# Kernel tuning notes

Measured on AMD Instinct MI355X. Metric: run time of the kernel, lower is better.

Reference implementation:

```python
import jax, jax.numpy as jnp
import numpy as np
import math

NUM_HEADS = 16


def setup_inputs() -> dict:
    key = jax.random.key(0)
    ks = jax.random.split(key, 7)
    d_model = 2048
    b, s = 2, 2048
    h = NUM_HEADS
    dh = d_model // h
    past_len = 2048
    std = math.sqrt(2.0 / (d_model + d_model))
    def w(k):
        return std * jax.random.truncated_normal(k, -3.0, 3.0, (d_model, d_model), jnp.float32)
    return {
        "x": jax.random.normal(ks[0], (b, s, d_model), jnp.float32),
        "past_k": jax.random.normal(ks[1], (b * h, past_len, dh), jnp.float32),
        "past_v": jax.random.normal(ks[2], (b * h, past_len, dh), jnp.float32),
        "Wq": w(ks[3]),
        "Wk": w(ks[4]),
        "Wv": w(ks[5]),
        "Wo": w(ks[6]),
    }


def reference(x, past_k, past_v, Wq, Wk, Wv, Wo):
    b, s, d_model = x.shape
    h = NUM_HEADS
    dh = d_model // h

    def proj_split(W):
        # (b, s, d_model) -> (b*h, s, dh)
        y = jnp.einsum('bsd,od->bso', x, W)
        return y.reshape(b, s, h, dh).transpose(0, 2, 1, 3).reshape(b * h, s, dh)

    Q = proj_split(Wq)
    K = proj_split(Wk)
    V = proj_split(Wv)

    past_len = past_k.shape[1]
    K = jnp.concatenate([past_k, K], axis=1)  # (b*h, total, dh)
    V = jnp.concatenate([past_v, V], axis=1)
    total = past_len + s

    # causal mask: query i (absolute pos past_len+i) attends to keys j <= past_len+i
    qi = jnp.arange(s)[:, None]
    kj = jnp.arange(total)[None, :]
    mask = kj <= (qi + past_len)  # (s, total)

    scores = jnp.einsum('bqd,bkd->bqk', Q, K) / math.sqrt(dh)
    scores = jnp.where(mask[None], scores, -jnp.inf)
    weights = jax.nn.softmax(scores, axis=-1)
    attn = jnp.einsum('bqk,bkv->bqv', weights, V)  # (b*h, s, dh)

    attn = attn.reshape(b, h, s, dh).transpose(0, 2, 1, 3).reshape(b, s, d_model)
    out = jnp.einsum('bsd,od->bso', attn, Wo)
    return out, K, V
```

## Files before the change

### kernel.cpp

```cpp
#include <hip/hip_runtime.h>

#define DM    2048
#define PAST  2048
#define TOT   4096
#define SCALE 0.08838834764831845f
#define QSCALE 0.1275475036480354f

typedef __attribute__((ext_vector_type(8))) short bf16x8;
typedef __attribute__((ext_vector_type(4))) float f32x4;
typedef __attribute__((ext_vector_type(4))) short s16x4;

typedef __attribute__((address_space(1))) void gvoid;
typedef __attribute__((address_space(3))) void lvoid;

__device__ __forceinline__ void gload16(const void* g, void* l) {
  __builtin_amdgcn_global_load_lds((gvoid*)g, (lvoid*)l, 16, 0, 0);
}

__device__ __forceinline__ short f2b(float f) {
  unsigned u = __float_as_uint(f);
  u += 0x7fffu + ((u >> 16) & 1u);
  return (short)(u >> 16);
}

__device__ __forceinline__ unsigned cvtpk(float lo, float hi) {
  unsigned r;
  asm("v_cvt_pk_bf16_f32 %0, %1, %2" : "=v"(r) : "v"(lo), "v"(hi));
  return r;
}

__device__ __forceinline__ float exp2hw(float x) {
  float r;
  asm("v_exp_f32 %0, %1" : "=v"(r) : "v"(x));
  return r;
}

template <bool F>
__device__ __forceinline__ bf16x8 ld8(const void* base, size_t eidx) {
  if constexpr (F) {
    const float* p = (const float*)base + eidx;
    float4 a = *(const float4*)p;
    float4 b = *(const float4*)(p + 4);
    union { unsigned u[4]; bf16x8 v; } r;
    r.u[0] = cvtpk(a.x, a.y); r.u[1] = cvtpk(a.z, a.w);
    r.u[2] = cvtpk(b.x, b.y); r.u[3] = cvtpk(b.z, b.w);
    return r.v;
  } else {
    return *(const bf16x8*)((const short*)base + eidx);
  }
}

__global__ void detect_dtype(const unsigned short* __restrict__ w, int* flag) {
  int cnt = 0;
#pragma unroll
  for (int i = 0; i < 4; ++i) {
    unsigned short v = w[i * 64 + threadIdx.x];
    int e = (v >> 7) & 0xFF;
    cnt += (e >= 126) ? 1 : 0;
  }
  for (int off = 32; off; off >>= 1) cnt += __shfl_down(cnt, off);
  if (threadIdx.x == 0) *flag = (cnt >= 8) ? 1 : 0;
}

__global__ __launch_bounds__(256)
void to_bf16(const int* __restrict__ flag,
             const float* __restrict__ x,
             const float* __restrict__ wq, const float* __restrict__ wk,
             const float* __restrict__ wv, const float* __restrict__ wo,
             short* __restrict__ xb, short* __restrict__ wqb,
             short* __restrict__ wkb, short* __restrict__ wvb,
             short* __restrict__ wob) {
  if (*flag != 1) return;
  const float* src; short* dst; size_t off = 0;
  switch (blockIdx.z) {
    case 0: src = x;  dst = xb;  break;
    case 1: src = x;  dst = xb;  off = 4194304; break;
    case 2: src = wq; dst = wqb; break;
    case 3: src = wk; dst = wkb; break;
    case 4: src = wv; dst = wvb; break;
    default: src = wo; dst = wob; break;
  }
  const size_t i = off + ((size_t)blockIdx.x * 256 + threadIdx.x) * 8;
  *(bf16x8*)(dst + i) = ld8<true>(src, i);
}

__device__ __forceinline__ void gemm_mainloop(
    const short* __restrict__ Ab, const short* __restrict__ Wb,
    short* sA, short* sB, f32x4 acc[4][4]) {
  const int tid  = threadIdx.x;
  const int lane = tid & 63, wid = tid >> 6;
  const int ln = lane & 15, qd = lane >> 4;
  const int wr = wid >> 1, wc = wid & 1;

  const int srow = lane >> 3;
  const int scol = ((lane & 7) ^ (lane >> 3)) * 8;

  auto stage = [&](int k0, int buf) {
#pragma unroll
    for (int i = 0; i < 4; ++i) {
      const int r8 = (wid * 4 + i) * 8 + srow;
      gload16(Ab + (size_t)r8 * DM + k0 + scol,
              (char*)sA + buf * 16384 + (wid * 4 + i) * 1024);
      gload16(Wb + (size_t)r8 * DM + k0 + scol,
              (char*)sB + buf * 16384 + (wid * 4 + i) * 1024);
    }
  };

  stage(0, 0);
  asm volatile("s_waitcnt vmcnt(0)" ::: "memory");
  __builtin_amdgcn_s_barrier();

  int cur = 0;
  for (int k0 = 0; k0 < DM; k0 += 64) {
    if (k0 + 64 < DM) stage(k0 + 64, cur ^ 1);

    const char* Ac = (const char*)sA + cur * 16384;
    const char* Bc = (const char*)sB + cur * 16384;
#pragma unroll
    for (int t = 0; t < 2; ++t) {
      bf16x8 af[4], bw[4];
#pragma unroll
      for (int i = 0; i < 4; ++i) {
        const int rowA = wr * 64 + i * 16 + ln;
        const int rowB = wc * 64 + i * 16 + ln;
        const int cb   = ((t << 2) + qd) << 4;
        af[i] = *(const bf16x8*)(Ac + rowA * 128 + (cb ^ ((rowA & 7) << 4)));
        bw[i] = *(const bf16x8*)(Bc + rowB * 128 + (cb ^ ((rowB & 7) << 4)));
      }
#pragma unroll
      for (int i = 0; i < 4; ++i)
#pragma unroll
        for (int j = 0; j < 4; ++j)
          acc[i][j] = __builtin_amdgcn_mfma_f32_16x16x32_bf16(af[i], bw[j], acc[i][j], 0, 0, 0);
    }
    asm volatile("s_waitcnt vmcnt(0)" ::: "memory");
    __builtin_amdgcn_s_barrier();
    cur ^= 1;
  }
}

__global__ __launch_bounds__(256, 2)
void qkv_gemm(const int* __restrict__ flag,
              const short* __restrict__ x0, const short* __restrict__ x1,
              const short* __restrict__ wq0, const short* __restrict__ wk0,
              const short* __restrict__ wv0,
              const short* __restrict__ wq1, const short* __restrict__ wk1,
              const short* __restrict__ wv1,
              short* __restrict__ Qws,
              short* __restrict__ Kb, float* __restrict__ Kf,
              short* __restrict__ Vb, float* __restrict__ Vf) {
  __shared__ __align__(16) short shA[2 * 128 * 64];
  __shared__ __align__(16) short shB[2 * 128 * 64];
  const int isF = *flag;
  const int bm = blockIdx.y, bn = blockIdx.x;
  const int seg = bn >> 4, bnl = bn & 15;

  const short* A = isF ? x1 : x0;
  const short* W = (seg == 0) ? (isF ? wq1 : wq0)
                  : (seg == 1) ? (isF ? wk1 : wk0)
                               : (isF ? wv1 : wv0);

  const f32x4 fz = {0.f, 0.f, 0.f, 0.f};
  f32x4 acc[4][4];
#pragma unroll
  for (int i = 0; i < 4; ++i)
#pragma unroll
    for (int j = 0; j < 4; ++j) acc[i][j] = fz;

  gemm_mainloop(A + (size_t)bm * 128 * DM, W + (size_t)bnl * 128 * DM, shA, shB, acc);

  const int tid  = threadIdx.x;
  const int lane = tid & 63, wid = tid >> 6;
  const int ln = lane & 15, qd = lane >> 4;
  const int wr = wid >> 1, wc = wid & 1;

#pragma unroll
  for (int i = 0; i < 4; ++i) {
    const int rbase = bm * 128 + wr * 64 + i * 16 + qd * 4;
#pragma unroll
    for (int j = 0; j < 4; ++j) {
      const int col = bnl * 128 + wc * 64 + j * 16 + ln;
#pragma unroll
      for (int r = 0; r < 4; ++r) {
        const int rr = rbase + r;
        const int bb = rr >> 11, sq = rr & 2047;
        const int hh = col >> 7, dd = col & 127;
        float v = acc[i][j][r];
        if (seg == 0) {
          const size_t idx = (((size_t)bb * 16 + hh) * 2048 + sq) * 128 + dd;
          Qws[idx] = f2b(v * QSCALE);
        } else {
          const size_t idx = (((size_t)bb * 16 + hh) * (size_t)TOT + PAST + sq) * 128 + dd;
          if (seg == 1) { if (isF) Kf[idx] = v; else Kb[idx] = f2b(v); }
          else          { if (isF) Vf[idx] = v; else Vb[idx] = f2b(v); }
        }
      }
    }
  }
}

__global__ __launch_bounds__(256, 2)
void out_gemm(const int* __restrict__ flag,
              const short* __restrict__ A,
              const short* __restrict__ wo0, const short* __restrict__ wo1,
              void* __restrict__ dst) {
  __shared__ __align__(16) short shA[2 * 128 * 64];
  __shared__ __align__(16) short shB[2 * 128 * 64];
  const int isF = *flag;
  const int bm = blockIdx.y, bn = blockIdx.x;
  const short* W = isF ? wo1 : wo0;

  const f32x4 fz = {0.f, 0.f, 0.f, 0.f};
  f32x4 acc[4][4];
#pragma unroll
  for (int i = 0; i < 4; ++i)
#pragma unroll
    for (int j = 0; j < 4; ++j) acc[i][j] = fz;

  gemm_mainloop(A + (size_t)bm * 128 * DM, W + (size_t)bn * 128 * DM, shA, shB, acc);

  const int tid  = threadIdx.x;
  const int lane = tid & 63, wid = tid >> 6;
  const int ln = lane & 15, qd = lane >> 4;
  const int wr = wid >> 1, wc = wid & 1;

#pragma unroll
  for (int i = 0; i < 4; ++i) {
    const int rbase = bm * 128 + wr * 64 + i * 16 + qd * 4;
#pragma unroll
    for (int j = 0; j < 4; ++j) {
      const int col = bn * 128 + wc * 64 + j * 16 + ln;
#pragma unroll
      for (int r = 0; r < 4; ++r) {
        const size_t idx = (size_t)(rbase + r) * DM + col;
        if (isF) ((float*)dst)[idx] = acc[i][j][r];
        else     ((short*)dst)[idx] = f2b(acc[i][j][r]);
      }
    }
  }
}

__global__ __launch_bounds__(256)
void copy_past(const int* __restrict__ flag,
               const void* __restrict__ pk, const void* __restrict__ pv,
               short* __restrict__ Kb, float* __restrict__ Kf,
               short* __restrict__ Vb, float* __restrict__ Vf) {
  const int isF = *flag;
  const void* src = blockIdx.z ? pv : pk;
  const size_t c = (size_t)blockIdx.x * 256 + threadIdx.x;
  const size_t bh = c >> 15;
  const size_t rem = c & 32767;
  const size_t si = c * 8, di = bh * (size_t)TOT * 128 + rem * 8;
  if (isF) {
    float* dst = blockIdx.z ? Vf : Kf;
    const float* s = (const float*)src + si;
    float4 a = *(const float4*)s, b = *(const float4*)(s + 4);
    *(float4*)(dst + di) = a; *(float4*)(dst + di + 4) = b;
  } else {
    short* dst = blockIdx.z ? Vb : Kb;
    *(bf16x8*)(dst + di) = *(const bf16x8*)((const short*)src + si);
  }
}

__global__ __launch_bounds__(256)
void transpose_v(const int* __restrict__ flag,
                 const short* __restrict__ Vb, const float* __restrict__ Vf,
                 short* __restrict__ Vt) {
  __shared__ __align__(16) short sh[64 * 136];
  const int isF = *flag;
  const int tid = threadIdx.x;
  const int bh = blockIdx.y, kb = blockIdx.x << 6;
  const int krow = tid >> 4, dc = tid & 15;
#pragma unroll
  for (int rnd = 0; rnd < 4; ++rnd) {
    const int key = rnd * 16 + krow;
    const size_t idx = ((size_t)bh * TOT + kb + key) * 128 + dc * 8;
    bf16x8 v = isF ? ld8<true>(Vf, idx) : ld8<false>(Vb, idx);
    *(bf16x8*)(sh + key * 136 + dc * 8) = v;
  }
  __syncthreads();
  short* dstb = Vt + (size_t)bh * 128 * TOT + kb;
  const int drow = tid >> 3, keyc = tid & 7;
#pragma unroll
  for (int rnd = 0; rnd < 4; ++rnd) {
    const int dr = rnd * 32 + drow;
    bf16x8 ov;
#pragma unroll
    for (int e = 0; e < 8; ++e) ov[e] = sh[(keyc * 8 + e) * 136 + dr];
    *(bf16x8*)(dstb + (size_t)dr * TOT + keyc * 8) = ov;
  }
}

template <bool F>
__global__ __launch_bounds__(256, 2)
void attn_kernel(const int* __restrict__ flag, int want,
                 const short* __restrict__ Q,
                 const void* __restrict__ K,
                 const short* __restrict__ Vt,
                 short* __restrict__ attn) {
  if (*flag != want) return;
  __shared__ __align__(16) short shK[64 * 136];
  __shared__ __align__(16) short shV[128 * 72];
  __shared__ __align__(16) short shP[4][32 * 72];

  const int tid = threadIdx.x;
  const int lane = tid & 63, wid = tid >> 6;
  const int ln = lane & 15, qd = lane >> 4;

  const int l = blockIdx.y * 16 + blockIdx.x;
  const int s = l >> 3;
  const int qt = (s < 32) ? (s >> 2) : (15 - ((s - 32) >> 2));
  const int bh = ((l & 7) << 2) | (s & 3);
  const int q0 = qt << 7;
  const int r0w = q0 + wid * 32;

  bf16x8 qf[2][4];
#pragma unroll
  for (int mi = 0; mi < 2; ++mi) {
    const short* Qb = Q + ((size_t)bh * 2048 + r0w + mi * 16 + ln) * 128;
#pragma unroll
    for (int t = 0; t < 4; ++t) qf[mi][t] = *(const bf16x8*)(Qb + t * 32 + qd * 8);
  }

  const f32x4 fz = {0.f, 0.f, 0.f, 0.f};
  f32x4 O[2][8];
#pragma unroll
  for (int mi = 0; mi < 2; ++mi)
#pragma unroll
    for (int dt = 0; dt < 8; ++dt) O[mi][dt] = fz;
  float m_i[2] = {-1e30f, -1e30f}, l_i[2] = {0.f, 0.f};

  const short* Vb = Vt + (size_t)bh * 128 * TOT;
  const int ntiles = 34 + 2 * qt;

  const int krow = tid >> 4, kcol = tid & 15;
  const int vrow = tid >> 3, vcol = tid & 7;
  short* shPw = &shP[wid][0];

  bf16x8 vk[4], vv[4];
#pragma unroll
  for (int rnd = 0; rnd < 4; ++rnd) {
    vk[rnd] = ld8<F>(K, ((size_t)bh * TOT + rnd * 16 + krow) * 128 + kcol * 8);
    vv[rnd] = *(const bf16x8*)(Vb + (size_t)(rnd * 32 + vrow) * TOT + vcol * 8);
  }

  for (int kt = 0; kt < ntiles; ++kt) {
    const int kb = kt << 6;
#pragma unroll
    for (int rnd = 0; rnd < 4; ++rnd) {
      *(bf16x8*)(shK + (rnd * 16 + krow) * 136 + kcol * 8) = vk[rnd];
      *(bf16x8*)(shV + (rnd * 32 + vrow) * 72 + vcol * 8) = vv[rnd];
    }
    __syncthreads();

    if (kt + 1 < ntiles) {
      const int nb = kb + 64;
#pragma unroll
      for (int rnd = 0; rnd < 4; ++rnd) {
        vk[rnd] = ld8<F>(K, ((size_t)bh * TOT + nb + rnd * 16 + krow) * 128 + kcol * 8);
        vv[rnd] = *(const bf16x8*)(Vb + (size_t)(rnd * 32 + vrow) * TOT + nb + vcol * 8);
      }
    }

    f32x4 sacc[2][4];
#pragma unroll
    for (int mi = 0; mi < 2; ++mi)
#pragma unroll
      for (int j = 0; j < 4; ++j) sacc[mi][j] = fz;
#pragma unroll
    for (int t = 0; t < 4; ++t) {
#pragma unroll
      for (int j = 0; j < 4; ++j) {
        bf16x8 kf = *(const bf16x8*)(shK + (j * 16 + ln) * 136 + ((t << 2) + qd) * 8);
        sacc[0][j] = __builtin_amdgcn_mfma_f32_16x16x32_bf16(kf, qf[0][t], sacc[0][j], 0, 0, 0);
        sacc[1][j] = __builtin_amdgcn_mfma_f32_16x16x32_bf16(kf, qf[1][t], sacc[1][j], 0, 0, 0);
      }
    }

    const bool maskt = (kt >= ntiles - 2);

#pragma unroll
    for (int mi = 0; mi < 2; ++mi) {
      const int q = r0w + mi * 16 + ln;
      float vmax = -1e30f;
      if (maskt) {
        const int lim = PAST + q;
#pragma unroll
        for (int j = 0; j < 4; ++j)
#pragma unroll
          for (int r = 0; r < 4; ++r) {
            const int kj = kb + j * 16 + qd * 4 + r;
            float v = sacc[mi][j][r];
            v = (kj <= lim) ? v : -1e30f;
            sacc[mi][j][r] = v;
            vmax = fmaxf(vmax, v);
          }
      } else {
#pragma unroll
        for (int j = 0; j < 4; ++j)
#pragma unroll
          for (int r = 0; r < 4; ++r) vmax = fmaxf(vmax, sacc[mi][j][r]);
      }
      vmax = fmaxf(vmax, __shfl_xor(vmax, 16));
      vmax = fmaxf(vmax, __shfl_xor(vmax, 32));
      const float mold = m_i[mi];
      const bool renew = vmax > mold + 8.0f;
      const float mnew = renew ? vmax : mold;
      float rsum = 0.f;
#pragma unroll
      for (int j = 0; j < 4; ++j)
#pragma unroll
        for (int r = 0; r < 4; ++r) {
          const float p = exp2hw(sacc[mi][j][r] - mnew);
          sacc[mi][j][r] = p;
          rsum += p;
        }
      rsum += __shfl_xor(rsum, 16);
      rsum += __shfl_xor(rsum, 32);
      if (renew) {
        const float alpha = exp2hw(mold - mnew);
        m_i[mi] = mnew;
        l_i[mi] = l_i[mi] * alpha + rsum;
#pragma unroll
        for (int dt = 0; dt < 8; ++dt) O[mi][dt] *= alpha;
      } else {
        l_i[mi] += rsum;
      }
      const int qr = mi * 16 + ln;
#pragma unroll
      for (int j = 0; j < 4; ++j) {
        uint2 w;
        w.x = cvtpk(sacc[mi][j][0], sacc[mi][j][1]);
        w.y = cvtpk(sacc[mi][j][2], sacc[mi][j][3]);
        *(uint2*)(shPw + qr * 72 + j * 16 + qd * 4) = w;
      }
    }

#pragma unroll
    for (int tk = 0; tk < 2; ++tk) {
      bf16x8 pf[2];
#pragma unroll
      for (int mi = 0; mi < 2; ++mi)
        pf[mi] = *(const bf16x8*)(shPw + (mi * 16 + ln) * 72 + ((tk << 2) + qd) * 8);
#pragma unroll
      for (int dt = 0; dt < 8; ++dt) {
        bf16x8 vf = *(const bf16x8*)(shV + (dt * 16 + ln) * 72 + ((tk << 2) + qd) * 8);
        O[0][dt] = __builtin_amdgcn_mfma_f32_16x16x32_bf16(vf, pf[0], O[0][dt], 0, 0, 0);
        O[1][dt] = __builtin_amdgcn_mfma_f32_16x16x32_bf16(vf, pf[1], O[1][dt], 0, 0, 0);
      }
    }
    __syncthreads();
  }

  const int bb = bh >> 4, hh = bh & 15;
#pragma unroll
  for (int mi = 0; mi < 2; ++mi) {
    const float inv = 1.0f / l_i[mi];
    const int q = r0w + mi * 16 + ln;
    short* dst = attn + ((size_t)bb * 2048 + q) * DM + hh * 128;
#pragma unroll
    for (int dt = 0; dt < 8; ++dt) {
      union { unsigned u[2]; s16x4 v; } o;
      o.u[0] = cvtpk(O[mi][dt][0] * inv, O[mi][dt][1] * inv);
      o.u[1] = cvtpk(O[mi][dt][2] * inv, O[mi][dt][3] * inv);
      *(s16x4*)(dst + dt * 16 + qd * 4) = o.v;
    }
  }
}

extern "C" void kernel_launch(void* const* d_in, const int* in_sizes, int n_in,
                              void* d_out, int out_size, void* d_ws, size_t ws_size,
                              hipStream_t stream) {
  (void)in_sizes; (void)n_in; (void)out_size; (void)ws_size;
  const void* x  = d_in[0];
  const void* pk = d_in[1];
  const void* pv = d_in[2];
  const void* Wq = d_in[3];
  const void* Wk = d_in[4];
  const void* Wv = d_in[5];
  const void* Wo = d_in[6];

  int* flag = (int*)d_ws;
  short* base = (short*)((char*)d_ws + 256);
  short* Qws    = base;
  short* attnws = base + 8388608;
  short* xb     = attnws;
  short* Vtws   = base + 16777216;
  short* wqb    = Vtws;
  short* wkb    = Vtws + 4194304;
  short* wvb    = Vtws + 8388608;
  short* wob    = base + 33554432;

  short* outB  = (short*)d_out;
  short* KoutB = outB + (size_t)8388608;
  short* VoutB = KoutB + (size_t)16777216;
  float* outF  = (float*)d_out;
  float* KoutF = outF + (size_t)8388608;
  float* VoutF = KoutF + (size_t)16777216;

  dim3 blk(256);
  detect_dtype<<<1, 64, 0, stream>>>((const unsigned short*)Wq, flag);

  to_bf16<<<dim3(2048, 1, 6), blk, 0, stream>>>(flag,
      (const float*)x, (const float*)Wq, (const float*)Wk, (const float*)Wv,
      (const float*)Wo, xb, wqb, wkb, wvb, wob);

  qkv_gemm<<<dim3(48, 32), blk, 0, stream>>>(flag,
      (const short*)x, xb,
      (const short*)Wq, (const short*)Wk, (const short*)Wv,
      wqb, wkb, wvb,
      Qws, KoutB, KoutF, VoutB, VoutF);

  copy_past<<<dim3(4096, 1, 2), blk, 0, stream>>>(flag, pk, pv,
      KoutB, KoutF, VoutB, VoutF);

  transpose_v<<<dim3(64, 32), blk, 0, stream>>>(flag, VoutB, VoutF, Vtws);

  attn_kernel<false><<<dim3(16, 32), blk, 0, stream>>>(flag, 0, Qws, KoutB, Vtws, attnws);
  attn_kernel<true ><<<dim3(16, 32), blk, 0, stream>>>(flag, 1, Qws, KoutF, Vtws, attnws);

  out_gemm<<<dim3(16, 32), blk, 0, stream>>>(flag, attnws,
      (const short*)Wo, wob, d_out);
}
```

Measured before the change: 658.5 us.

## Use 256x256 tiles with 512 threads and XCD-aware block remap in QKV GEMM

The QKV projection GEMM moves from 128x128 tiles with 256 threads to 256x256 tiles with 8 waves, each computing a 128x64 sub-tile. A 1D grid is remapped so neighbouring tiles land on the same XCD, aiming for better L2 reuse. Larger tiles raise data reuse per LDS load but cut the block count to 384, which risks poor wave balance across CUs and higher register pressure. The old mainloop is kept for the output GEMM, with its barriers switched to __syncthreads.

```diff
diff --git a/kernel.cpp b/kernel.cpp
--- a/kernel.cpp
+++ b/kernel.cpp
@@ -84,62 +84,58 @@
   *(bf16x8*)(dst + i) = ld8<true>(src, i);
 }
 
-__device__ __forceinline__ void gemm_mainloop(
+__device__ __forceinline__ void gemm256_mainloop(
     const short* __restrict__ Ab, const short* __restrict__ Wb,
-    short* sA, short* sB, f32x4 acc[4][4]) {
-  const int tid  = threadIdx.x;
+    short* sA, short* sB, f32x4 acc[8][4]) {
+  const int tid = threadIdx.x;
   const int lane = tid & 63, wid = tid >> 6;
   const int ln = lane & 15, qd = lane >> 4;
-  const int wr = wid >> 1, wc = wid & 1;
-
-  const int srow = lane >> 3;
-  const int scol = ((lane & 7) ^ (lane >> 3)) * 8;
+  const int wm = wid >> 2, wn = wid & 3;
 
   auto stage = [&](int k0, int buf) {
 #pragma unroll
     for (int i = 0; i < 4; ++i) {
-      const int r8 = (wid * 4 + i) * 8 + srow;
-      gload16(Ab + (size_t)r8 * DM + k0 + scol,
-              (char*)sA + buf * 16384 + (wid * 4 + i) * 1024);
-      gload16(Wb + (size_t)r8 * DM + k0 + scol,
-              (char*)sB + buf * 16384 + (wid * 4 + i) * 1024);
+      const int c = i * 512 + tid;
+      const int row = c >> 3;
+      const int sc = (c & 7) ^ (row & 7);
+      gload16(Ab + (size_t)row * DM + k0 + sc * 8,
+              (char*)sA + buf * 32768 + c * 16);
+      gload16(Wb + (size_t)row * DM + k0 + sc * 8,
+              (char*)sB + buf * 32768 + c * 16);
     }
   };
 
   stage(0, 0);
-  asm volatile("s_waitcnt vmcnt(0)" ::: "memory");
-  __builtin_amdgcn_s_barrier();
-
-  int cur = 0;
-  for (int k0 = 0; k0 < DM; k0 += 64) {
-    if (k0 + 64 < DM) stage(k0 + 64, cur ^ 1);
-
-    const char* Ac = (const char*)sA + cur * 16384;
-    const char* Bc = (const char*)sB + cur * 16384;
-#pragma unroll
-    for (int t = 0; t < 2; ++t) {
-      bf16x8 af[4], bw[4];
-#pragma unroll
-      for (int i = 0; i < 4; ++i) {
-        const int rowA = wr * 64 + i * 16 + ln;
-        const int rowB = wc * 64 + i * 16 + ln;
-        const int cb   = ((t << 2) + qd) << 4;
-        af[i] = *(const bf16x8*)(Ac + rowA * 128 + (cb ^ ((rowA & 7) << 4)));
-        bw[i] = *(const bf16x8*)(Bc + rowB * 128 + (cb ^ ((rowB & 7) << 4)));
-      }
-#pragma unroll
-      for (int i = 0; i < 4; ++i)
+  __syncthreads();
+
+  for (int t = 0; t < 32; ++t) {
+    if (t + 1 < 32) stage((t + 1) * 64, (t + 1) & 1);
+    const char* Ac = (const char*)sA + (t & 1) * 32768;
+    const char* Bc = (const char*)sB + (t & 1) * 32768;
+#pragma unroll
+    for (int h = 0; h < 2; ++h) {
+      bf16x8 af[8], bw[4];
+#pragma unroll
+      for (int j = 0; j < 4; ++j) {
+        const int row = wn * 64 + j * 16 + ln;
+        bw[j] = *(const bf16x8*)(Bc + row * 128 + (((h * 4 + qd) ^ (row & 7)) * 16));
+      }
+#pragma unroll
+      for (int i = 0; i < 8; ++i) {
+        const int row = wm * 128 + i * 16 + ln;
+        af[i] = *(const bf16x8*)(Ac + row * 128 + (((h * 4 + qd) ^ (row & 7)) * 16));
+      }
+#pragma unroll
+      for (int i = 0; i < 8; ++i)
 #pragma unroll
         for (int j = 0; j < 4; ++j)
           acc[i][j] = __builtin_amdgcn_mfma_f32_16x16x32_bf16(af[i], bw[j], acc[i][j], 0, 0, 0);
     }
-    asm volatile("s_waitcnt vmcnt(0)" ::: "memory");
-    __builtin_amdgcn_s_barrier();
-    cur ^= 1;
-  }
-}
-
-__global__ __launch_bounds__(256, 2)
+    __syncthreads();
+  }
+}
+
+__global__ __launch_bounds__(512, 2)
 void qkv_gemm(const int* __restrict__ flag,
               const short* __restrict__ x0, const short* __restrict__ x1,
               const short* __restrict__ wq0, const short* __restrict__ wk0,
@@ -149,37 +145,40 @@
               short* __restrict__ Qws,
               short* __restrict__ Kb, float* __restrict__ Kf,
               short* __restrict__ Vb, float* __restrict__ Vf) {
-  __shared__ __align__(16) short shA[2 * 128 * 64];
-  __shared__ __align__(16) short shB[2 * 128 * 64];
+  __shared__ __align__(16) short sA[2 * 256 * 64];
+  __shared__ __align__(16) short sB[2 * 256 * 64];
   const int isF = *flag;
-  const int bm = blockIdx.y, bn = blockIdx.x;
-  const int seg = bn >> 4, bnl = bn & 15;
-
-  const short* A = isF ? x1 : x0;
-  const short* W = (seg == 0) ? (isF ? wq1 : wq0)
-                  : (seg == 1) ? (isF ? wk1 : wk0)
-                               : (isF ? wv1 : wv0);
+
+  const int orig = blockIdx.x;
+  const int wg = (orig & 7) * 48 + (orig >> 3);
+  const int bm = wg / 24, bn = wg % 24;
+  const int seg = bn >> 3, bnl = bn & 7;
+
+  const short* A = (isF ? x1 : x0) + (size_t)bm * 256 * DM;
+  const short* W = ((seg == 0) ? (isF ? wq1 : wq0)
+                   : (seg == 1) ? (isF ? wk1 : wk0)
+                                : (isF ? wv1 : wv0)) + (size_t)bnl * 256 * DM;
 
   const f32x4 fz = {0.f, 0.f, 0.f, 0.f};
-  f32x4 acc[4][4];
-#pragma unroll
-  for (int i = 0; i < 4; ++i)
+  f32x4 acc[8][4];
+#pragma unroll
+  for (int i = 0; i < 8; ++i)
 #pragma unroll
     for (int j = 0; j < 4; ++j) acc[i][j] = fz;
 
-  gemm_mainloop(A + (size_t)bm * 128 * DM, W + (size_t)bnl * 128 * DM, shA, shB, acc);
-
-  const int tid  = threadIdx.x;
+  gemm256_mainloop(A, W, sA, sB, acc);
+
+  const int tid = threadIdx.x;
   const int lane = tid & 63, wid = tid >> 6;
   const int ln = lane & 15, qd = lane >> 4;
-  const int wr = wid >> 1, wc = wid & 1;
-
-#pragma unroll
-  for (int i = 0; i < 4; ++i) {
-    const int rbase = bm * 128 + wr * 64 + i * 16 + qd * 4;
+  const int wm = wid >> 2, wn = wid & 3;
+
+#pragma unroll
+  for (int i = 0; i < 8; ++i) {
+    const int rbase = bm * 256 + wm * 128 + i * 16 + qd * 4;
 #pragma unroll
     for (int j = 0; j < 4; ++j) {
-      const int col = bnl * 128 + wc * 64 + j * 16 + ln;
+      const int col = bnl * 256 + wn * 64 + j * 16 + ln;
 #pragma unroll
       for (int r = 0; r < 4; ++r) {
         const int rr = rbase + r;
@@ -196,6 +195,56 @@
         }
       }
     }
+  }
+}
+
+__device__ __forceinline__ void gemm_mainloop(
+    const short* __restrict__ Ab, const short* __restrict__ Wb,
+    short* sA, short* sB, f32x4 acc[4][4]) {
+  const int tid  = threadIdx.x;
+  const int lane = tid & 63, wid = tid >> 6;
+  const int ln = lane & 15, qd = lane >> 4;
+  const int wr = wid >> 1, wc = wid & 1;
+
+  const int srow = lane >> 3;
+  const int scol = ((lane & 7) ^ (lane >> 3)) * 8;
+
+  auto stage = [&](int k0, int buf) {
+#pragma unroll
+    for (int i = 0; i < 4; ++i) {
+      const int r8 = (wid * 4 + i) * 8 + srow;
+      gload16(Ab + (size_t)r8 * DM + k0 + scol,
+              (char*)sA + buf * 16384 + (wid * 4 + i) * 1024);
+      gload16(Wb + (size_t)r8 * DM + k0 + scol,
+              (char*)sB + buf * 16384 + (wid * 4 + i) * 1024);
+    }
+  };
+
+  stage(0, 0);
+  __syncthreads();
+
+  for (int k0 = 0; k0 < DM; k0 += 64) {
+    if (k0 + 64 < DM) stage(k0 + 64, ((k0 >> 6) + 1) & 1);
+    const char* Ac = (const char*)sA + ((k0 >> 6) & 1) * 16384;
+    const char* Bc = (const char*)sB + ((k0 >> 6) & 1) * 16384;
+#pragma unroll
+    for (int t = 0; t < 2; ++t) {
+      bf16x8 af[4], bw[4];
+#pragma unroll
+      for (int i = 0; i < 4; ++i) {
+        const int rowA = wr * 64 + i * 16 + ln;
+        const int rowB = wc * 64 + i * 16 + ln;
+        const int cb   = ((t << 2) + qd) << 4;
+        af[i] = *(const bf16x8*)(Ac + rowA * 128 + (cb ^ ((rowA & 7) << 4)));
+        bw[i] = *(const bf16x8*)(Bc + rowB * 128 + (cb ^ ((rowB & 7) << 4)));
+      }
+#pragma unroll
+      for (int i = 0; i < 4; ++i)
+#pragma unroll
+        for (int j = 0; j < 4; ++j)
+          acc[i][j] = __builtin_amdgcn_mfma_f32_16x16x32_bf16(af[i], bw[j], acc[i][j], 0, 0, 0);
+    }
+    __syncthreads();
   }
 }
 
@@ -505,7 +554,7 @@
       (const float*)x, (const float*)Wq, (const float*)Wk, (const float*)Wv,
       (const float*)Wo, xb, wqb, wkb, wvb, wob);
 
-  qkv_gemm<<<dim3(48, 32), blk, 0, stream>>>(flag,
+  qkv_gemm<<<dim3(384), dim3(512), 0, stream>>>(flag,
       (const short*)x, xb,
       (const short*)Wq, (const short*)Wk, (const short*)Wv,
       wqb, wkb, wvb,
```

Measured after the change: 695.6 us. +5.6%, slower.
